# Kernel optimization log

Measured on AMD Instinct MI355X. Metric: run time of the kernel, lower is better.

## Reference

```python
import jax, jax.numpy as jnp
import numpy as np

B, T, D, C = 64, 512, 768, 31  # batch, bert seq len, hidden size, num clause boundaries


def setup_inputs() -> dict:
    key = jax.random.key(0)
    k1, k2, k3 = jax.random.split(key, 3)
    hidden_state = jax.random.normal(k1, (B, T, D), dtype=jnp.float32)
    # Strictly increasing clause-end token positions in (0, T): evenly spaced base + jitter
    step = T // (C + 1)  # 16
    base = (jnp.arange(1, C + 1) * step)[None, :]                       # [1, C]
    jitter = jax.random.randint(k2, (B, C), 0, step - 1)                # < step => strictly increasing
    clause_b = (base + jitter).astype(jnp.int32)                        # [B, C]
    w5 = jax.random.normal(k3, (D, 1), dtype=jnp.float32) * 0.02        # fc5 weight
    b5 = jnp.zeros((1,), dtype=jnp.float32)                             # fc5 bias
    return {"hidden_state": hidden_state, "clause_b": clause_b, "w5": w5, "b5": b5}


def reference(hidden_state, clause_b, w5, b5):
    # Per-clause variable-length softmax-attention pooling over BERT hidden states.
    # Segment j of batch b covers tokens [starts[b,j], ends[b,j]).
    Bq, Tq, Dq = hidden_state.shape
    scores = (hidden_state @ w5).squeeze(-1) + b5[0]                    # [B, T]  (fc5)
    starts = jnp.concatenate(
        [jnp.zeros((Bq, 1), clause_b.dtype), clause_b], axis=1)        # [B, C+1]
    ends = jnp.concatenate(
        [clause_b, jnp.full((Bq, 1), Tq, clause_b.dtype)], axis=1)     # [B, C+1]
    t = jnp.arange(Tq)
    mask = (t[None, None, :] >= starts[:, :, None]) & \
           (t[None, None, :] < ends[:, :, None])                       # [B, C+1, T]
    neg = jnp.asarray(-1e30, dtype=scores.dtype)
    s = jnp.where(mask, scores[:, None, :], neg)
    w = jax.nn.softmax(s, axis=-1)                                      # [B, C+1, T]
    doc_sents_h = jnp.einsum('bjt,btd->bjd', w, hidden_state)           # [B, C+1, D]
    return doc_sents_h
```

## Files before the change

### kernel.cpp

```cpp
#include <hip/hip_runtime.h>


#define B_ 64
#define T_ 512
#define D_ 768
#define C_ 31
#define NSEG 32

__global__ __launch_bounds__(256) void seg_softmax_pool_split(
    const float* __restrict__ hidden,
    const int*   __restrict__ clause_b,
    const float* __restrict__ w5,
    const float* __restrict__ b5,
    float*       __restrict__ out)
{
    const int tid  = threadIdx.x;
    const int wave = tid >> 6;
    const int lane = tid & 63;
    const int seg  = blockIdx.x;
    const int b    = seg >> 5;
    const int j    = seg & 31;

    const int start = (j == 0)  ? 0  : clause_b[b * C_ + j - 1];
    const int end   = (j == C_) ? T_ : clause_b[b * C_ + j];
    const int L     = end - start;

    const int doff = 4 * lane;
    const float4 w0 = *(const float4*)(w5 + doff);
    const float4 w1 = *(const float4*)(w5 + doff + 256);
    const float4 w2 = *(const float4*)(w5 + doff + 512);
    const float bias = b5[0];

    const float* hseg = hidden + ((size_t)b * T_ + start) * D_ + doff;

    float4 a0 = make_float4(0.f, 0.f, 0.f, 0.f);
    float4 a1 = a0, a2 = a0;
    float m = -INFINITY, denom = 0.0f;

    float4 c0 = a0, c1 = a0, c2 = a0;
    if (wave < L) {
        const float* p0 = hseg + (size_t)wave * D_;
        c0 = *(const float4*)(p0);
        c1 = *(const float4*)(p0 + 256);
        c2 = *(const float4*)(p0 + 512);
    }

    for (int t = wave; t < L; t += 4) {
        float4 n0 = make_float4(0.f, 0.f, 0.f, 0.f), n1 = n0, n2 = n0;
        if (t + 4 < L) {
            const float* np = hseg + (size_t)(t + 4) * D_;
            n0 = *(const float4*)(np);
            n1 = *(const float4*)(np + 256);
            n2 = *(const float4*)(np + 512);
        }

        float p = c0.x * w0.x + c0.y * w0.y + c0.z * w0.z + c0.w * w0.w
                + c1.x * w1.x + c1.y * w1.y + c1.z * w1.z + c1.w * w1.w
                + c2.x * w2.x + c2.y * w2.y + c2.z * w2.z + c2.w * w2.w;
        #pragma unroll
        for (int off = 32; off > 0; off >>= 1)
            p += __shfl_xor(p, off, 64);
        const float s = p + bias;

        const float mn    = fmaxf(m, s);
        const float scale = __expf(m - mn);
        const float e     = __expf(s - mn);
        denom = denom * scale + e;
        a0.x = a0.x * scale + e * c0.x;  a0.y = a0.y * scale + e * c0.y;
        a0.z = a0.z * scale + e * c0.z;  a0.w = a0.w * scale + e * c0.w;
        a1.x = a1.x * scale + e * c1.x;  a1.y = a1.y * scale + e * c1.y;
        a1.z = a1.z * scale + e * c1.z;  a1.w = a1.w * scale + e * c1.w;
        a2.x = a2.x * scale + e * c2.x;  a2.y = a2.y * scale + e * c2.y;
        a2.z = a2.z * scale + e * c2.z;  a2.w = a2.w * scale + e * c2.w;
        m = mn;
        c0 = n0; c1 = n1; c2 = n2;
    }

    __shared__ float s_acc[4][D_];
    __shared__ float s_m[4], s_d[4];

    if (lane == 0) { s_m[wave] = m; s_d[wave] = denom; }
    __syncthreads();

    const float M = fmaxf(fmaxf(s_m[0], s_m[1]), fmaxf(s_m[2], s_m[3]));
    const float Tden = s_d[0] * __expf(s_m[0] - M) + s_d[1] * __expf(s_m[1] - M)
                     + s_d[2] * __expf(s_m[2] - M) + s_d[3] * __expf(s_m[3] - M);
    const float myscale = __expf(m - M);

    float* dst = &s_acc[wave][doff];
    *(float4*)(dst)       = make_float4(a0.x * myscale, a0.y * myscale, a0.z * myscale, a0.w * myscale);
    *(float4*)(dst + 256) = make_float4(a1.x * myscale, a1.y * myscale, a1.z * myscale, a1.w * myscale);
    *(float4*)(dst + 512) = make_float4(a2.x * myscale, a2.y * myscale, a2.z * myscale, a2.w * myscale);
    __syncthreads();

    const float inv = 1.0f / Tden;
    float* op = out + ((size_t)b * NSEG + j) * D_;
    #pragma unroll
    for (int k = 0; k < 3; ++k) {
        const int d = tid + k * 256;
        const float v = s_acc[0][d] + s_acc[1][d] + s_acc[2][d] + s_acc[3][d];
        op[d] = v * inv;
    }
}

extern "C" void kernel_launch(void* const* d_in, const int* in_sizes, int n_in,
                              void* d_out, int out_size, void* d_ws, size_t ws_size,
                              hipStream_t stream) {
    const float* hidden   = (const float*)d_in[0];
    const int*   clause_b = (const int*)d_in[1];
    const float* w5       = (const float*)d_in[2];
    const float* b5       = (const float*)d_in[3];
    float*       out      = (float*)d_out;

    seg_softmax_pool_split<<<B_ * NSEG, 256, 0, stream>>>(hidden, clause_b, w5, b5, out);
}
```

Before: 155.1 us.

## Replace online softmax with two-pass score-then-weighted-sum segment pooling

```diff
diff --git a/kernel.cpp b/kernel.cpp
--- a/kernel.cpp
+++ b/kernel.cpp
@@ -7,7 +7,7 @@
 #define C_ 31
 #define NSEG 32
 
-__global__ __launch_bounds__(256) void seg_softmax_pool_split(
+__global__ __launch_bounds__(256) void seg_softmax_pool_2p(
     const float* __restrict__ hidden,
     const int*   __restrict__ clause_b,
     const float* __restrict__ w5,
@@ -29,77 +29,62 @@
     const float4 w0 = *(const float4*)(w5 + doff);
     const float4 w1 = *(const float4*)(w5 + doff + 256);
     const float4 w2 = *(const float4*)(w5 + doff + 512);
-    const float bias = b5[0];
 
     const float* hseg = hidden + ((size_t)b * T_ + start) * D_ + doff;
 
-    float4 a0 = make_float4(0.f, 0.f, 0.f, 0.f);
-    float4 a1 = a0, a2 = a0;
-    float m = -INFINITY, denom = 0.0f;
+    __shared__ float s_s[NSEG];
+    __shared__ float s_acc[4][D_];
 
-    float4 c0 = a0, c1 = a0, c2 = a0;
-    if (wave < L) {
-        const float* p0 = hseg + (size_t)wave * D_;
-        c0 = *(const float4*)(p0);
-        c1 = *(const float4*)(p0 + 256);
-        c2 = *(const float4*)(p0 + 512);
-    }
-
+    #pragma unroll 2
     for (int t = wave; t < L; t += 4) {
-        float4 n0 = make_float4(0.f, 0.f, 0.f, 0.f), n1 = n0, n2 = n0;
-        if (t + 4 < L) {
-            const float* np = hseg + (size_t)(t + 4) * D_;
-            n0 = *(const float4*)(np);
-            n1 = *(const float4*)(np + 256);
-            n2 = *(const float4*)(np + 512);
-        }
-
-        float p = c0.x * w0.x + c0.y * w0.y + c0.z * w0.z + c0.w * w0.w
+        const float* p = hseg + (size_t)t * D_;
+        const float4 c0 = *(const float4*)(p);
+        const float4 c1 = *(const float4*)(p + 256);
+        const float4 c2 = *(const float4*)(p + 512);
+        float s = c0.x * w0.x + c0.y * w0.y + c0.z * w0.z + c0.w * w0.w
                 + c1.x * w1.x + c1.y * w1.y + c1.z * w1.z + c1.w * w1.w
                 + c2.x * w2.x + c2.y * w2.y + c2.z * w2.z + c2.w * w2.w;
         #pragma unroll
         for (int off = 32; off > 0; off >>= 1)
-            p += __shfl_xor(p, off, 64);
-        const float s = p + bias;
+            s += __shfl_xor(s, off, 64);
+        if (lane == 0) s_s[t] = s;
+    }
+    __syncthreads();
 
-        const float mn    = fmaxf(m, s);
-        const float scale = __expf(m - mn);
-        const float e     = __expf(s - mn);
-        denom = denom * scale + e;
-        a0.x = a0.x * scale + e * c0.x;  a0.y = a0.y * scale + e * c0.y;
-        a0.z = a0.z * scale + e * c0.z;  a0.w = a0.w * scale + e * c0.w;
-        a1.x = a1.x * scale + e * c1.x;  a1.y = a1.y * scale + e * c1.y;
-        a1.z = a1.z * scale + e * c1.z;  a1.w = a1.w * scale + e * c1.w;
-        a2.x = a2.x * scale + e * c2.x;  a2.y = a2.y * scale + e * c2.y;
-        a2.z = a2.z * scale + e * c2.z;  a2.w = a2.w * scale + e * c2.w;
-        m = mn;
-        c0 = n0; c1 = n1; c2 = n2;
+    float M = -INFINITY;
+    for (int t = 0; t < L; ++t) M = fmaxf(M, s_s[t]);
+    float S = 0.0f;
+    for (int t = 0; t < L; ++t) S += __expf(s_s[t] - M);
+    const float invS = 1.0f / S;
+
+    float4 a0 = make_float4(0.f, 0.f, 0.f, 0.f);
+    float4 a1 = a0, a2 = a0;
+    #pragma unroll 2
+    for (int t = wave; t < L; t += 4) {
+        const float wgt = __expf(s_s[t] - M) * invS;
+        const float* p = hseg + (size_t)t * D_;
+        const float4 c0 = *(const float4*)(p);
+        const float4 c1 = *(const float4*)(p + 256);
+        const float4 c2 = *(const float4*)(p + 512);
+        a0.x = fmaf(wgt, c0.x, a0.x);  a0.y = fmaf(wgt, c0.y, a0.y);
+        a0.z = fmaf(wgt, c0.z, a0.z);  a0.w = fmaf(wgt, c0.w, a0.w);
+        a1.x = fmaf(wgt, c1.x, a1.x);  a1.y = fmaf(wgt, c1.y, a1.y);
+        a1.z = fmaf(wgt, c1.z, a1.z);  a1.w = fmaf(wgt, c1.w, a1.w);
+        a2.x = fmaf(wgt, c2.x, a2.x);  a2.y = fmaf(wgt, c2.y, a2.y);
+        a2.z = fmaf(wgt, c2.z, a2.z);  a2.w = fmaf(wgt, c2.w, a2.w);
     }
 
-    __shared__ float s_acc[4][D_];
-    __shared__ float s_m[4], s_d[4];
-
-    if (lane == 0) { s_m[wave] = m; s_d[wave] = denom; }
+    float* dst = &s_acc[wave][doff];
+    *(float4*)(dst)       = a0;
+    *(float4*)(dst + 256) = a1;
+    *(float4*)(dst + 512) = a2;
     __syncthreads();
 
-    const float M = fmaxf(fmaxf(s_m[0], s_m[1]), fmaxf(s_m[2], s_m[3]));
-    const float Tden = s_d[0] * __expf(s_m[0] - M) + s_d[1] * __expf(s_m[1] - M)
-                     + s_d[2] * __expf(s_m[2] - M) + s_d[3] * __expf(s_m[3] - M);
-    const float myscale = __expf(m - M);
-
-    float* dst = &s_acc[wave][doff];
-    *(float4*)(dst)       = make_float4(a0.x * myscale, a0.y * myscale, a0.z * myscale, a0.w * myscale);
-    *(float4*)(dst + 256) = make_float4(a1.x * myscale, a1.y * myscale, a1.z * myscale, a1.w * myscale);
-    *(float4*)(dst + 512) = make_float4(a2.x * myscale, a2.y * myscale, a2.z * myscale, a2.w * myscale);
-    __syncthreads();
-
-    const float inv = 1.0f / Tden;
     float* op = out + ((size_t)b * NSEG + j) * D_;
     #pragma unroll
     for (int k = 0; k < 3; ++k) {
         const int d = tid + k * 256;
-        const float v = s_acc[0][d] + s_acc[1][d] + s_acc[2][d] + s_acc[3][d];
-        op[d] = v * inv;
+        op[d] = s_acc[0][d] + s_acc[1][d] + s_acc[2][d] + s_acc[3][d];
     }
 }
 
@@ -112,5 +97,5 @@
     const float* b5       = (const float*)d_in[3];
     float*       out      = (float*)d_out;
 
-    seg_softmax_pool_split<<<B_ * NSEG, 256, 0, stream>>>(hidden, clause_b, w5, b5, out);
+    seg_softmax_pool_2p<<<B_ * NSEG, 256, 0, stream>>>(hidden, clause_b, w5, b5, out);
 }
```

Measured after the change: 160.9 us. 3.7% more time.
